# Kernel tuning notes

Hardware: AMD Instinct MI355X
Metric: run time of the kernel (lower is better)

The kernel has to match this reference:

```python
import jax, jax.numpy as jnp
import numpy as np

B, N, C, H = 2, 2048, 1024, 16
D = C // H  # head_dim = 64
EPS = 1e-6


def _rope_freqs(n, d):
    inv_freq = 1.0 / (10000.0 ** (np.arange(0, d // 2, dtype=np.float32) * 2.0 / d))
    ang = np.arange(n, dtype=np.float32)[:, None] * inv_freq[None, :]  # [N, D/2]
    ang = np.concatenate([ang, ang], axis=-1)  # [N, D] (chunk-in-half convention)
    cos = jnp.asarray(np.cos(ang))[None, None]  # [1,1,N,D]
    sin = jnp.asarray(np.sin(ang))[None, None]
    return cos, sin


def setup_inputs() -> dict:
    key = jax.random.key(0)
    k1, k2, k3 = jax.random.split(key, 3)
    x = jax.random.normal(k1, (B, N, C), dtype=jnp.float32)
    w_qkv = jax.random.normal(k2, (3 * C, C), dtype=jnp.float32) * (C ** -0.5)
    w_proj = jax.random.normal(k3, (C, C), dtype=jnp.float32) * (C ** -0.5)
    b_proj = jnp.zeros((C,), dtype=jnp.float32)
    freqs_cos, freqs_sin = _rope_freqs(N, D)
    return {"x": x, "w_qkv": w_qkv, "w_proj": w_proj, "b_proj": b_proj,
            "freqs_cos": freqs_cos, "freqs_sin": freqs_sin}


def _layernorm(t):
    # affine-free LayerNorm over the last (head_dim) axis
    mu = jnp.mean(t, axis=-1, keepdims=True)
    var = jnp.var(t, axis=-1, keepdims=True)
    return (t - mu) * jax.lax.rsqrt(var + EPS)


def _rotate_half(t):
    t1, t2 = jnp.split(t, 2, axis=-1)
    return jnp.concatenate([-t2, t1], axis=-1)


def reference(x, w_qkv, w_proj, b_proj, freqs_cos, freqs_sin):
    b, n, c = x.shape
    qkv = jnp.einsum('bnc,kc->bnk', x, w_qkv)  # [B,N,3C]
    qkv = qkv.reshape(b, n, 3, H, D).transpose(2, 0, 3, 1, 4)  # [3,B,H,N,D]
    q, k, v = qkv[0], qkv[1], qkv[2]
    q = _layernorm(q)
    k = _layernorm(k)
    q = q * freqs_cos + _rotate_half(q) * freqs_sin
    k = k * freqs_cos + _rotate_half(k) * freqs_sin
    scale = D ** -0.5
    scores = jnp.einsum('bhqd,bhkd->bhqk', q, k) * scale  # [B,H,N,N]
    attn = jax.nn.softmax(scores, axis=-1)
    out = jnp.einsum('bhqk,bhkd->bhqd', attn, v)  # [B,H,N,D]
    out = out.transpose(0, 2, 1, 3).reshape(b, n, c)
    return jnp.einsum('bnc,oc->bno', out, w_proj) + b_proj
```

## Files before the change

kernel.cpp:

```cpp
#include <hip/hip_runtime.h>
#include <hip/hip_bf16.h>


typedef __bf16 bf16x8 __attribute__((ext_vector_type(8)));
typedef float f32x4 __attribute__((ext_vector_type(4)));
typedef float f32x16 __attribute__((ext_vector_type(16)));
typedef unsigned short us8 __attribute__((ext_vector_type(8)));
typedef unsigned short us4 __attribute__((ext_vector_type(4)));

static __device__ __forceinline__ unsigned short f2b(float f) {
  __hip_bfloat16 h = __float2bfloat16(f);
  return __builtin_bit_cast(unsigned short, h);
}
static __device__ __forceinline__ float b2f(unsigned short u) {
  __hip_bfloat16 h = __builtin_bit_cast(__hip_bfloat16, u);
  return __bfloat162float(h);
}

#if __has_builtin(__builtin_amdgcn_exp2f)
static __device__ __forceinline__ float fast_exp2(float x) { return __builtin_amdgcn_exp2f(x); }
#else
static __device__ __forceinline__ float fast_exp2(float x) { return exp2f(x); }
#endif

static __device__ __forceinline__ void async_copy16(void* lds, const void* g) {
  __builtin_amdgcn_global_load_lds(
      (const __attribute__((address_space(1))) void*)g,
      (__attribute__((address_space(3))) void*)lds, 16, 0, 0);
}

static __device__ __forceinline__ unsigned cvt_pk_bf16(float lo, float hi) {
  unsigned r;
  asm("v_cvt_pk_bf16_f32 %0, %1, %2" : "=v"(r) : "v"(lo), "v"(hi));
  return r;
}
static __device__ __forceinline__ void swap32(unsigned& x, unsigned& y) {
  asm("v_permlane32_swap_b32 %0, %1" : "+v"(x), "+v"(y));
}
static __device__ __forceinline__ float max3f(float a, float b, float c) {
  float d;
  asm("v_max3_f32 %0, %1, %2, %3" : "=v"(d) : "v"(a), "v"(b), "v"(c));
  return d;
}
static __device__ __forceinline__ float vmax16(const f32x16& v) {
  float a = max3f(v[0], v[1], v[2]);
  float b = max3f(v[3], v[4], v[5]);
  float c = max3f(v[6], v[7], v[8]);
  float d = max3f(v[9], v[10], v[11]);
  float e = max3f(v[12], v[13], v[14]);
  float x = max3f(a, b, c);
  float y = max3f(d, e, v[15]);
  return fmaxf(x, y);
}

__global__ __launch_bounds__(256) void cvt_all(
    const float* __restrict__ x, const float* __restrict__ wqkv,
    const float* __restrict__ wproj, unsigned short* __restrict__ x_bf,
    unsigned short* __restrict__ wqkv_bf, unsigned short* __restrict__ wproj_bf) {
  int i = blockIdx.x * 256 + threadIdx.x;
  const float* src;
  unsigned short* dst;
  int off;
  if (i < 524288) {
    src = x; dst = x_bf; off = i;
  } else if (i < 917504) {
    src = wqkv; dst = wqkv_bf; off = i - 524288;
  } else {
    src = wproj; dst = wproj_bf; off = i - 917504;
  }
  const float4* p = reinterpret_cast<const float4*>(src) + (size_t)off * 2;
  float4 a = p[0], b = p[1];
  us8 v;
  v[0] = f2b(a.x); v[1] = f2b(a.y); v[2] = f2b(a.z); v[3] = f2b(a.w);
  v[4] = f2b(b.x); v[5] = f2b(b.y); v[6] = f2b(b.z); v[7] = f2b(b.w);
  reinterpret_cast<us8*>(dst)[off] = v;
}

__global__ __launch_bounds__(256, 3) void gemm_qkv(
    const unsigned short* __restrict__ A,
    const unsigned short* __restrict__ Bw,
    const float* __restrict__ fcos, const float* __restrict__ fsin,
    unsigned short* __restrict__ qo, unsigned short* __restrict__ ko,
    unsigned short* __restrict__ vt)
{
  __shared__ unsigned short a_sh[128 * 64];
  __shared__ unsigned short b_sh[128 * 64];
  const int tid = threadIdx.x;
  const int lane = tid & 63;
  const int w = tid >> 6;
  const int wr = w >> 1, wc = w & 1;
  const int l15 = lane & 15, l4 = lane >> 4;
  const int m0 = blockIdx.y * 128;
  const int n0 = blockIdx.x * 128;
  const int r8 = lane >> 3, c8 = lane & 7;
  const int K = 1024;

  f32x4 acc[4][4] = {};

  for (int k0 = 0; k0 < K; k0 += 64) {
#pragma unroll
    for (int p = 0; p < 8; ++p) {
      int s = p * 4 + w;
      if (s < 16) {
        int row = s * 8 + r8;
        async_copy16(&a_sh[s * 512],
                     &A[(size_t)(m0 + row) * K + k0 + ((c8 ^ (row & 7)) << 3)]);
      } else {
        int s2 = s - 16;
        int row = s2 * 8 + r8;
        async_copy16(&b_sh[s2 * 512],
                     &Bw[(size_t)(n0 + row) * K + k0 + ((c8 ^ (row & 7)) << 3)]);
      }
    }
    __syncthreads();
#pragma unroll
    for (int kk = 0; kk < 2; ++kk) {
      bf16x8 af[4], bfr[4];
#pragma unroll
      for (int mf = 0; mf < 4; ++mf) {
        int r = wr * 64 + mf * 16 + l15;
        af[mf] = *reinterpret_cast<const bf16x8*>(
            &a_sh[r * 64 + (((kk * 4 + l4) ^ (r & 7)) << 3)]);
      }
#pragma unroll
      for (int nf = 0; nf < 4; ++nf) {
        int r = wc * 64 + nf * 16 + l15;
        bfr[nf] = *reinterpret_cast<const bf16x8*>(
            &b_sh[r * 64 + (((kk * 4 + l4) ^ (r & 7)) << 3)]);
      }
#pragma unroll
      for (int mf = 0; mf < 4; ++mf)
#pragma unroll
        for (int nf = 0; nf < 4; ++nf)
          acc[mf][nf] = __builtin_amdgcn_mfma_f32_16x16x32_bf16(af[mf], bfr[nf], acc[mf][nf], 0, 0, 0);
    }
    __syncthreads();
  }

  const int colbase = n0 + wc * 64;
  const int three = colbase >> 10;
  const int hh = (colbase >> 6) & 15;
  const int b_ = m0 >> 11;
  const int nbase = (m0 & 2047) + wr * 64;
  unsigned short* ep = ((w < 2) ? a_sh : b_sh) + (w & 1) * 4096;
  const int cch = lane & 7, rb2 = lane >> 3;

  if (three < 2) {
    const float sc = three ? 1.f : 0.18033688011112042f;
#pragma unroll
    for (int mf = 0; mf < 4; ++mf) {
#pragma unroll
      for (int j = 0; j < 4; ++j) {
        float a0 = acc[mf][0][j], a1 = acc[mf][1][j];
        float a2 = acc[mf][2][j], a3 = acc[mf][3][j];
        float s1 = (a0 + a1) + (a2 + a3);
        float s2 = (a0 * a0 + a1 * a1) + (a2 * a2 + a3 * a3);
#pragma unroll
        for (int off = 8; off; off >>= 1) {
          s1 += __shfl_xor(s1, off);
          s2 += __shfl_xor(s2, off);
        }
        float mu = s1 * (1.f / 64.f);
        float inv = rsqrtf(s2 * (1.f / 64.f) - mu * mu + 1e-6f);
        int rloc = mf * 16 + l4 * 4 + j;
        int n = nbase + rloc;
        const float* cp = &fcos[(size_t)n * 64];
        const float* sp = &fsin[(size_t)n * 64];
#pragma unroll
        for (int nf = 0; nf < 4; ++nf) {
          int d = nf * 16 + l15;
          float tt = (acc[mf][nf][j] - mu) * inv;
          float tp = (acc[mf][nf ^ 2][j] - mu) * inv;
          float r = sc * (tt * cp[d] + ((nf < 2) ? -tp : tp) * sp[d]);
          ep[rloc * 64 + ((((d >> 3) ^ (rloc & 7)) << 3) | (d & 7))] = f2b(r);
        }
      }
    }
    unsigned short* dst =
        (three ? ko : qo) + (size_t)(b_ * 16 + hh) * 2048 * 64;
#pragma unroll
    for (int i = 0; i < 8; ++i) {
      int row = i * 8 + rb2;
      us8 vd = *reinterpret_cast<const us8*>(
          &ep[row * 64 + ((cch ^ (row & 7)) << 3)]);
      *reinterpret_cast<us8*>(&dst[(size_t)(nbase + row) * 64 + cch * 8]) = vd;
    }
  } else {
#pragma unroll
    for (int mf = 0; mf < 4; ++mf)
#pragma unroll
      for (int nf = 0; nf < 4; ++nf) {
        int d = nf * 16 + l15;
#pragma unroll
        for (int j = 0; j < 4; ++j) {
          int nl = mf * 16 + l4 * 4 + j;
          ep[d * 64 + ((((nl >> 3) ^ (d & 7)) << 3) | (nl & 7))] =
              f2b(acc[mf][nf][j]);
        }
      }
    unsigned short* dst = vt + (size_t)(b_ * 16 + hh) * 64 * 2048;
#pragma unroll
    for (int i = 0; i < 8; ++i) {
      int d = i * 8 + rb2;
      us8 vd = *reinterpret_cast<const us8*>(
          &ep[d * 64 + ((cch ^ (d & 7)) << 3)]);
      *reinterpret_cast<us8*>(&dst[(size_t)d * 2048 + nbase + cch * 8]) = vd;
    }
  }
}

__global__ __launch_bounds__(256, 2) void gemm_proj(
    const unsigned short* __restrict__ A, const unsigned short* __restrict__ Bw,
    const float* __restrict__ bias, float* __restrict__ Cout,
    int M, int Nn, int K) {
  __shared__ unsigned short a_sh[128 * 64];
  __shared__ unsigned short b_sh[64 * 64];
  const int tid = threadIdx.x;
  const int lane = tid & 63;
  const int w = tid >> 6;
  const int wr = w >> 1, wc = w & 1;
  const int l15 = lane & 15, l4 = lane >> 4;
  const int m0 = blockIdx.y * 128;
  const int n0 = blockIdx.x * 64;
  const int r8 = lane >> 3, c8 = lane & 7;

  f32x4 acc[4][2] = {};

  for (int k0 = 0; k0 < K; k0 += 64) {
#pragma unroll
    for (int p = 0; p < 6; ++p) {
      int s = p * 4 + w;
      if (s < 16) {
        int row = s * 8 + r8;
        async_copy16(&a_sh[s * 512],
                     &A[(size_t)(m0 + row) * K + k0 + ((c8 ^ (row & 7)) << 3)]);
      } else {
        int s2 = s - 16;
        int row = s2 * 8 + r8;
        async_copy16(&b_sh[s2 * 512],
                     &Bw[(size_t)(n0 + row) * K + k0 + ((c8 ^ (row & 7)) << 3)]);
      }
    }
    __syncthreads();
#pragma unroll
    for (int kk = 0; kk < 2; ++kk) {
      bf16x8 af[4], bfr[2];
#pragma unroll
      for (int mf = 0; mf < 4; ++mf) {
        int r = wr * 64 + mf * 16 + l15;
        af[mf] = *reinterpret_cast<const bf16x8*>(
            &a_sh[r * 64 + (((kk * 4 + l4) ^ (r & 7)) << 3)]);
      }
#pragma unroll
      for (int nf = 0; nf < 2; ++nf) {
        int r = wc * 32 + nf * 16 + l15;
        bfr[nf] = *reinterpret_cast<const bf16x8*>(
            &b_sh[r * 64 + (((kk * 4 + l4) ^ (r & 7)) << 3)]);
      }
#pragma unroll
      for (int mf = 0; mf < 4; ++mf)
#pragma unroll
        for (int nf = 0; nf < 2; ++nf)
          acc[mf][nf] = __builtin_amdgcn_mfma_f32_16x16x32_bf16(af[mf], bfr[nf], acc[mf][nf], 0, 0, 0);
    }
    __syncthreads();
  }
#pragma unroll
  for (int mf = 0; mf < 4; ++mf)
#pragma unroll
    for (int nf = 0; nf < 2; ++nf) {
      int col = n0 + wc * 32 + nf * 16 + l15;
#pragma unroll
      for (int j = 0; j < 4; ++j) {
        int row = m0 + wr * 64 + mf * 16 + l4 * 4 + j;
        Cout[(size_t)row * Nn + col] = acc[mf][nf][j] + bias[col];
      }
    }
}

__global__ __launch_bounds__(256, 2) void attn_kern(
    const unsigned short* __restrict__ Q,
    const unsigned short* __restrict__ Kk,
    const unsigned short* __restrict__ Vt,
    unsigned short* __restrict__ O)
{
  __shared__ unsigned short k_sh[2][128 * 64];
  __shared__ unsigned short v_sh[2][64 * 128];
  const int tid = threadIdx.x;
  const int lane = tid & 63;
  const int w = tid >> 6;
  const int l31 = lane & 31;
  const int H = lane >> 5;
  const int bid = blockIdx.x;
  const int wid = (bid & 7) * 64 + (bid >> 3);
  const int qt = wid & 15;
  const int bh = wid >> 4;
  const int h = bh & 15, b = bh >> 4;
  const unsigned short* qb = Q + (size_t)bh * 2048 * 64;
  const unsigned short* kb = Kk + (size_t)bh * 2048 * 64;
  const unsigned short* vb = Vt + (size_t)bh * 64 * 2048;
  const int tok = qt * 128 + w * 32 + l31;

  bf16x8 qf[4];
#pragma unroll
  for (int c = 0; c < 4; ++c)
    qf[c] = *reinterpret_cast<const bf16x8*>(&qb[(size_t)tok * 64 + c * 16 + H * 8]);

  f32x16 oT[2] = {};
  float mr = -1e30f, lr = 0.f;

  const int r8 = lane >> 3, cc8 = lane & 7;
  const int r4 = lane >> 4, cc16 = lane & 15;
#define ATTN_STAGE(KT, BUF)                                                           \
  {                                                                                   \
    _Pragma("unroll") for (int p = 0; p < 8; ++p) {                                   \
      int sseg = p * 4 + w;                                                           \
      if (sseg < 16) {                                                                \
        int row = sseg * 8 + r8;                                                      \
        async_copy16(&k_sh[BUF][sseg * 512],                                          \
                     &kb[(size_t)((KT) * 128 + row) * 64 + ((cc8 ^ (row & 7)) << 3)]);   \
      } else {                                                                        \
        int s2 = sseg - 16;                                                           \
        int row = s2 * 4 + r4;                                                        \
        async_copy16(&v_sh[BUF][s2 * 512],                                            \
                     &vb[(size_t)row * 2048 + (KT) * 128 + ((cc16 ^ (row & 7)) << 3)]);  \
      }                                                                               \
    }                                                                                 \
  }

  ATTN_STAGE(0, 0);
  __syncthreads();

  for (int kt = 0; kt < 16; ++kt) {
    const int cur = kt & 1;
    if (kt < 15) ATTN_STAGE(kt + 1, cur ^ 1);

#pragma unroll
    for (int sub = 0; sub < 2; ++sub) {
      f32x16 sT[2] = {};
#pragma unroll
      for (int c = 0; c < 4; ++c) {
        int ch0 = 2 * c + H;
#pragma unroll
        for (int t = 0; t < 2; ++t) {
          int r = (sub * 2 + t) * 32 + l31;
          bf16x8 ka = *reinterpret_cast<const bf16x8*>(
              &k_sh[cur][r * 64 + ((ch0 ^ (r & 7)) << 3)]);
          sT[t] = __builtin_amdgcn_mfma_f32_32x32x16_bf16(ka, qf[c], sT[t], 0, 0, 0);
        }
      }
      float tmax = fmaxf(vmax16(sT[0]), vmax16(sT[1]));
      tmax = fmaxf(tmax, __shfl_xor(tmax, 32));
      if (__any(tmax > mr + 8.f)) {
        float mn = fmaxf(mr, tmax);
        float corr = fast_exp2(mr - mn);
        mr = mn;
        lr *= corr;
#pragma unroll
        for (int r = 0; r < 16; ++r) { oT[0][r] *= corr; oT[1][r] *= corr; }
      }
      float tsum = 0.f;
#pragma unroll
      for (int t = 0; t < 2; ++t)
#pragma unroll
        for (int r = 0; r < 16; ++r) {
          float p = fast_exp2(sT[t][r] - mr);
          sT[t][r] = p;
          tsum += p;
        }
      lr += tsum;

      bf16x8 pB[4];
#pragma unroll
      for (int t = 0; t < 2; ++t)
#pragma unroll
        for (int half = 0; half < 2; ++half) {
          const int base = 8 * half;
          unsigned x0 = cvt_pk_bf16(sT[t][base + 0], sT[t][base + 1]);
          unsigned x1 = cvt_pk_bf16(sT[t][base + 2], sT[t][base + 3]);
          unsigned y0 = cvt_pk_bf16(sT[t][base + 4], sT[t][base + 5]);
          unsigned y1 = cvt_pk_bf16(sT[t][base + 6], sT[t][base + 7]);
          swap32(x0, y0);
          swap32(x1, y1);
          int4 packed = {(int)x0, (int)x1, (int)y0, (int)y1};
          pB[2 * t + half] = __builtin_bit_cast(bf16x8, packed);
        }
#pragma unroll
      for (int dt = 0; dt < 2; ++dt) {
        int r = dt * 32 + l31;
#pragma unroll
        for (int mi = 0; mi < 4; ++mi) {
          int ch = (8 * sub + 2 * mi + H) ^ (r & 7);
          bf16x8 va = *reinterpret_cast<const bf16x8*>(&v_sh[cur][r * 128 + (ch << 3)]);
          oT[dt] = __builtin_amdgcn_mfma_f32_32x32x16_bf16(va, pB[mi], oT[dt], 0, 0, 0);
        }
      }
    }
    __syncthreads();
  }
  lr += __shfl_xor(lr, 32);
  float invl = 1.f / lr;
#pragma unroll
  for (int dt = 0; dt < 2; ++dt)
#pragma unroll
    for (int rb = 0; rb < 4; ++rb) {
      us4 ov;
#pragma unroll
      for (int j = 0; j < 4; ++j) ov[j] = f2b(oT[dt][rb * 4 + j] * invl);
      *reinterpret_cast<us4*>(
          &O[((size_t)b * 2048 + tok) * 1024 + h * 64 + 32 * dt + 8 * rb + 4 * H]) = ov;
    }
#undef ATTN_STAGE
}

extern "C" void kernel_launch(void* const* d_in, const int* in_sizes, int n_in,
                              void* d_out, int out_size, void* d_ws, size_t ws_size,
                              hipStream_t stream) {
  (void)in_sizes; (void)n_in; (void)out_size; (void)ws_size;
  const float* x      = (const float*)d_in[0];
  const float* w_qkv  = (const float*)d_in[1];
  const float* w_proj = (const float*)d_in[2];
  const float* b_proj = (const float*)d_in[3];
  const float* fcos   = (const float*)d_in[4];
  const float* fsin   = (const float*)d_in[5];
  float* out = (float*)d_out;
  char* ws = (char*)d_ws;

  unsigned short* x_bf     = (unsigned short*)(ws + 0);
  unsigned short* wqkv_bf  = (unsigned short*)(ws + 8388608);
  unsigned short* wproj_bf = (unsigned short*)(ws + 14680064);
  unsigned short* q_bf     = (unsigned short*)(ws + 16777216);
  unsigned short* k_bf     = (unsigned short*)(ws + 25165824);
  unsigned short* vt_bf    = (unsigned short*)(ws + 33554432);
  unsigned short* ao_bf    = (unsigned short*)(ws + 41943040);

  cvt_all<<<4096, 256, 0, stream>>>(x, w_qkv, w_proj, x_bf, wqkv_bf, wproj_bf);
  gemm_qkv<<<dim3(24, 32), 256, 0, stream>>>(x_bf, wqkv_bf, fcos, fsin,
                                             q_bf, k_bf, vt_bf);
  attn_kern<<<512, 256, 0, stream>>>(q_bf, k_bf, vt_bf, ao_bf);
  gemm_proj<<<dim3(16, 32), 256, 0, stream>>>(ao_bf, wproj_bf, b_proj, out,
                                              4096, 1024, 1024);
}
```

Before: 111.1 us.

## Process two 32-query tiles per wave in attention to reuse K/V fragments

Each wave in the attention kernel now handles 64 queries as two 32-row tiles. Each K and V fragment read from LDS therefore feeds two MFMAs, and the query tile per block grows from 128 to 256. This halves LDS reads and global K/V traffic per query and gives the scheduler two independent softmax streams to interleave. In exchange, register pressure roughly doubles, launch bounds drop to one block per SIMD, and the grid shrinks to 256 blocks, which is about one block per CU on mi355x and leaves less parallelism to hide latency.

New measurement: 121.4 us. 9.3% more time.

```diff
diff --git a/kernel.cpp b/kernel.cpp
--- a/kernel.cpp
+++ b/kernel.cpp
@@ -278,7 +278,7 @@
     }
 }
 
-__global__ __launch_bounds__(256, 2) void attn_kern(
+__global__ __launch_bounds__(256, 1) void attn_kern(
     const unsigned short* __restrict__ Q,
     const unsigned short* __restrict__ Kk,
     const unsigned short* __restrict__ Vt,
@@ -292,22 +292,26 @@
   const int l31 = lane & 31;
   const int H = lane >> 5;
   const int bid = blockIdx.x;
-  const int wid = (bid & 7) * 64 + (bid >> 3);
-  const int qt = wid & 15;
-  const int bh = wid >> 4;
+  const int wid = (bid & 7) * 32 + (bid >> 3);
+  const int qt = wid & 7;
+  const int bh = wid >> 3;
   const int h = bh & 15, b = bh >> 4;
   const unsigned short* qb = Q + (size_t)bh * 2048 * 64;
   const unsigned short* kb = Kk + (size_t)bh * 2048 * 64;
   const unsigned short* vb = Vt + (size_t)bh * 64 * 2048;
-  const int tok = qt * 128 + w * 32 + l31;
-
-  bf16x8 qf[4];
-#pragma unroll
-  for (int c = 0; c < 4; ++c)
-    qf[c] = *reinterpret_cast<const bf16x8*>(&qb[(size_t)tok * 64 + c * 16 + H * 8]);
-
-  f32x16 oT[2] = {};
-  float mr = -1e30f, lr = 0.f;
+  const int qbase = qt * 256 + w * 64;
+  const int tokA = qbase + l31;
+  const int tokB = qbase + 32 + l31;
+
+  bf16x8 qfA[4], qfB[4];
+#pragma unroll
+  for (int c = 0; c < 4; ++c) {
+    qfA[c] = *reinterpret_cast<const bf16x8*>(&qb[(size_t)tokA * 64 + c * 16 + H * 8]);
+    qfB[c] = *reinterpret_cast<const bf16x8*>(&qb[(size_t)tokB * 64 + c * 16 + H * 8]);
+  }
+
+  f32x16 oTA[2] = {}, oTB[2] = {};
+  float mrA = -1e30f, lrA = 0.f, mrB = -1e30f, lrB = 0.f;
 
   const int r8 = lane >> 3, cc8 = lane & 7;
   const int r4 = lane >> 4, cc16 = lane & 15;
@@ -328,6 +332,42 @@
     }                                                                                 \
   }
 
+#define SOFTMAX_PACK(sT, mr, lr, oT, pB)                                              \
+  {                                                                                   \
+    float tmax = fmaxf(vmax16(sT[0]), vmax16(sT[1]));                                 \
+    tmax = fmaxf(tmax, __shfl_xor(tmax, 32));                                         \
+    if (__any(tmax > mr + 8.f)) {                                                     \
+      float mn = fmaxf(mr, tmax);                                                     \
+      float corr = fast_exp2(mr - mn);                                                \
+      mr = mn;                                                                        \
+      lr *= corr;                                                                     \
+      _Pragma("unroll") for (int r = 0; r < 16; ++r) {                                \
+        oT[0][r] *= corr;                                                             \
+        oT[1][r] *= corr;                                                             \
+      }                                                                               \
+    }                                                                                 \
+    float tsum = 0.f;                                                                 \
+    _Pragma("unroll") for (int t = 0; t < 2; ++t)                                     \
+        _Pragma("unroll") for (int r = 0; r < 16; ++r) {                              \
+      float p = fast_exp2(sT[t][r] - mr);                                             \
+      sT[t][r] = p;                                                                   \
+      tsum += p;                                                                      \
+    }                                                                                 \
+    lr += tsum;                                                                       \
+    _Pragma("unroll") for (int t = 0; t < 2; ++t)                                     \
+        _Pragma("unroll") for (int half = 0; half < 2; ++half) {                      \
+      const int base = 8 * half;                                                      \
+      unsigned x0 = cvt_pk_bf16(sT[t][base + 0], sT[t][base + 1]);                    \
+      unsigned x1 = cvt_pk_bf16(sT[t][base + 2], sT[t][base + 3]);                    \
+      unsigned y0 = cvt_pk_bf16(sT[t][base + 4], sT[t][base + 5]);                    \
+      unsigned y1 = cvt_pk_bf16(sT[t][base + 6], sT[t][base + 7]);                    \
+      swap32(x0, y0);                                                                 \
+      swap32(x1, y1);                                                                 \
+      int4 packed = {(int)x0, (int)x1, (int)y0, (int)y1};                             \
+      pB[2 * t + half] = __builtin_bit_cast(bf16x8, packed);                          \
+    }                                                                                 \
+  }
+
   ATTN_STAGE(0, 0);
   __syncthreads();
 
@@ -337,54 +377,26 @@
 
 #pragma unroll
     for (int sub = 0; sub < 2; ++sub) {
-      f32x16 sT[2] = {};
-#pragma unroll
-      for (int c = 0; c < 4; ++c) {
-        int ch0 = 2 * c + H;
+      bf16x8 ka[8];
+#pragma unroll
+      for (int c = 0; c < 4; ++c)
 #pragma unroll
         for (int t = 0; t < 2; ++t) {
           int r = (sub * 2 + t) * 32 + l31;
-          bf16x8 ka = *reinterpret_cast<const bf16x8*>(
-              &k_sh[cur][r * 64 + ((ch0 ^ (r & 7)) << 3)]);
-          sT[t] = __builtin_amdgcn_mfma_f32_32x32x16_bf16(ka, qf[c], sT[t], 0, 0, 0);
-        }
-      }
-      float tmax = fmaxf(vmax16(sT[0]), vmax16(sT[1]));
-      tmax = fmaxf(tmax, __shfl_xor(tmax, 32));
-      if (__any(tmax > mr + 8.f)) {
-        float mn = fmaxf(mr, tmax);
-        float corr = fast_exp2(mr - mn);
-        mr = mn;
-        lr *= corr;
-#pragma unroll
-        for (int r = 0; r < 16; ++r) { oT[0][r] *= corr; oT[1][r] *= corr; }
-      }
-      float tsum = 0.f;
-#pragma unroll
-      for (int t = 0; t < 2; ++t)
-#pragma unroll
-        for (int r = 0; r < 16; ++r) {
-          float p = fast_exp2(sT[t][r] - mr);
-          sT[t][r] = p;
-          tsum += p;
-        }
-      lr += tsum;
-
-      bf16x8 pB[4];
-#pragma unroll
-      for (int t = 0; t < 2; ++t)
-#pragma unroll
-        for (int half = 0; half < 2; ++half) {
-          const int base = 8 * half;
-          unsigned x0 = cvt_pk_bf16(sT[t][base + 0], sT[t][base + 1]);
-          unsigned x1 = cvt_pk_bf16(sT[t][base + 2], sT[t][base + 3]);
-          unsigned y0 = cvt_pk_bf16(sT[t][base + 4], sT[t][base + 5]);
-          unsigned y1 = cvt_pk_bf16(sT[t][base + 6], sT[t][base + 7]);
-          swap32(x0, y0);
-          swap32(x1, y1);
-          int4 packed = {(int)x0, (int)x1, (int)y0, (int)y1};
-          pB[2 * t + half] = __builtin_bit_cast(bf16x8, packed);
-        }
+          ka[c * 2 + t] = *reinterpret_cast<const bf16x8*>(
+              &k_sh[cur][r * 64 + (((2 * c + H) ^ (r & 7)) << 3)]);
+        }
+      f32x16 sA[2] = {}, sB[2] = {};
+#pragma unroll
+      for (int c = 0; c < 4; ++c)
+#pragma unroll
+        for (int t = 0; t < 2; ++t) {
+          sA[t] = __builtin_amdgcn_mfma_f32_32x32x16_bf16(ka[c * 2 + t], qfA[c], sA[t], 0, 0, 0);
+          sB[t] = __builtin_amdgcn_mfma_f32_32x32x16_bf16(ka[c * 2 + t], qfB[c], sB[t], 0, 0, 0);
+        }
+      bf16x8 pbA[4], pbB[4];
+      SOFTMAX_PACK(sA, mrA, lrA, oTA, pbA);
+      SOFTMAX_PACK(sB, mrB, lrB, oTB, pbB);
 #pragma unroll
       for (int dt = 0; dt < 2; ++dt) {
         int r = dt * 32 + l31;
@@ -392,25 +404,32 @@
         for (int mi = 0; mi < 4; ++mi) {
           int ch = (8 * sub + 2 * mi + H) ^ (r & 7);
           bf16x8 va = *reinterpret_cast<const bf16x8*>(&v_sh[cur][r * 128 + (ch << 3)]);
-          oT[dt] = __builtin_amdgcn_mfma_f32_32x32x16_bf16(va, pB[mi], oT[dt], 0, 0, 0);
+          oTA[dt] = __builtin_amdgcn_mfma_f32_32x32x16_bf16(va, pbA[mi], oTA[dt], 0, 0, 0);
+          oTB[dt] = __builtin_amdgcn_mfma_f32_32x32x16_bf16(va, pbB[mi], oTB[dt], 0, 0, 0);
         }
       }
     }
     __syncthreads();
   }
-  lr += __shfl_xor(lr, 32);
-  float invl = 1.f / lr;
+  lrA += __shfl_xor(lrA, 32);
+  lrB += __shfl_xor(lrB, 32);
+  float invA = 1.f / lrA, invB = 1.f / lrB;
 #pragma unroll
   for (int dt = 0; dt < 2; ++dt)
 #pragma unroll
     for (int rb = 0; rb < 4; ++rb) {
-      us4 ov;
-#pragma unroll
-      for (int j = 0; j < 4; ++j) ov[j] = f2b(oT[dt][rb * 4 + j] * invl);
-      *reinterpret_cast<us4*>(
-          &O[((size_t)b * 2048 + tok) * 1024 + h * 64 + 32 * dt + 8 * rb + 4 * H]) = ov;
+      us4 ovA, ovB;
+#pragma unroll
+      for (int j = 0; j < 4; ++j) {
+        ovA[j] = f2b(oTA[dt][rb * 4 + j] * invA);
+        ovB[j] = f2b(oTB[dt][rb * 4 + j] * invB);
+      }
+      size_t dcol = h * 64 + 32 * dt + 8 * rb + 4 * H;
+      *reinterpret_cast<us4*>(&O[((size_t)b * 2048 + tokA) * 1024 + dcol]) = ovA;
+      *reinterpret_cast<us4*>(&O[((size_t)b * 2048 + tokB) * 1024 + dcol]) = ovB;
     }
 #undef ATTN_STAGE
+#undef SOFTMAX_PACK
 }
 
 extern "C" void kernel_launch(void* const* d_in, const int* in_sizes, int n_in,
@@ -437,7 +456,7 @@
   cvt_all<<<4096, 256, 0, stream>>>(x, w_qkv, w_proj, x_bf, wqkv_bf, wproj_bf);
   gemm_qkv<<<dim3(24, 32), 256, 0, stream>>>(x_bf, wqkv_bf, fcos, fsin,
                                              q_bf, k_bf, vt_bf);
-  attn_kern<<<512, 256, 0, stream>>>(q_bf, k_bf, vt_bf, ao_bf);
+  attn_kern<<<256, 256, 0, stream>>>(q_bf, k_bf, vt_bf, ao_bf);
   gemm_proj<<<dim3(16, 32), 256, 0, stream>>>(ao_bf, wproj_bf, b_proj, out,
                                               4096, 1024, 1024);
 }
```
